# Kernel optimization log

Hardware: AMD Instinct MI355X
Metric: run time of the kernel (lower is better)

The kernel has to match this reference:

```python
import jax, jax.numpy as jnp
import numpy as np

EPS = 1e-6
N_HEADS, N_POINTS = 6, 4


def layer_norm(x, w, b):
    m = jnp.mean(x, -1, keepdims=True)
    v = jnp.mean((x - m) ** 2, -1, keepdims=True)
    return (x - m) * jax.lax.rsqrt(v + EPS) * w + b


def bilinear_sample(val, loc, Hl, Wl):
    # val: (B, nH, Hl*Wl, d); loc: (B, Lq, nH, P, 2) in [0,1]
    # matches F.grid_sample(mode='bilinear', padding='zeros', align_corners=False)
    B, nH, _, d = val.shape
    Lq, P = loc.shape[1], loc.shape[3]
    x = loc[..., 0] * Wl - 0.5
    y = loc[..., 1] * Hl - 0.5
    x0 = jnp.floor(x)
    y0 = jnp.floor(y)
    wx1 = x - x0
    wy1 = y - y0
    out = jnp.zeros((B, nH, Lq * P, d), val.dtype)
    corners = ((0, 0, (1 - wy1) * (1 - wx1)), (0, 1, (1 - wy1) * wx1),
               (1, 0, wy1 * (1 - wx1)), (1, 1, wy1 * wx1))
    for dy, dx, w in corners:
        xi = x0 + dx
        yi = y0 + dy
        valid = (xi >= 0) & (xi < Wl) & (yi >= 0) & (yi < Hl)
        xi_c = jnp.clip(xi, 0, Wl - 1).astype(jnp.int32)
        yi_c = jnp.clip(yi, 0, Hl - 1).astype(jnp.int32)
        idx = (yi_c * Wl + xi_c).transpose(0, 2, 1, 3).reshape(B, nH, Lq * P)
        g = jnp.take_along_axis(val, idx[..., None], axis=2)  # (B,nH,Lq*P,d)
        ww = jnp.where(valid, w, 0.0).transpose(0, 2, 1, 3).reshape(B, nH, Lq * P)
        out = out + g * ww[..., None]
    return out.reshape(B, nH, Lq, P, d).transpose(0, 2, 1, 3, 4)  # (B,Lq,nH,P,d)


def dwconv3x3(x, w, b):
    # x: (N, C, H, W); w: (C, 1, 3, 3) depthwise
    y = jax.lax.conv_general_dilated(x, w, (1, 1), 'SAME',
                                     feature_group_count=w.shape[0],
                                     dimension_numbers=('NCHW', 'OIHW', 'NCHW'))
    return y + b[None, :, None, None]


def setup_inputs() -> dict:
    key = jax.random.key(0)
    ks = jax.random.split(key, 16)
    B, H, W, C = 8, 32, 32, 768
    Lq = 3 * H * W
    Hf = Wf = 64
    hidden = int(C * 0.25)
    s = 0.02
    inp = {
        'query': jax.random.normal(ks[0], (B, Lq, C), jnp.float32),
        'reference_points': jax.random.uniform(ks[1], (B, Lq, 1, 2), jnp.float32),
        'feat': jax.random.normal(ks[2], (B, Hf * Wf, C), jnp.float32),
        'spatial_shapes': jnp.array([[Hf, Wf]], jnp.int32),
        'level_start_index': jnp.zeros((1,), jnp.int32),
        'H': H, 'W': W,
        'qn_w': jnp.ones((C,)), 'qn_b': jnp.zeros((C,)),
        'fn_w': jnp.ones((C,)), 'fn_b': jnp.zeros((C,)),
        'so_w': jax.random.normal(ks[3], (C, N_HEADS * N_POINTS * 2)) * s,
        'so_b': jax.random.normal(ks[4], (N_HEADS * N_POINTS * 2,)) * s,
        'aw_w': jax.random.normal(ks[5], (C, N_HEADS * N_POINTS)) * s,
        'aw_b': jnp.zeros((N_HEADS * N_POINTS,)),
        'vp_w': jax.random.normal(ks[6], (C, C)) * s,
        'vp_b': jnp.zeros((C,)),
        'op_w': jax.random.normal(ks[7], (C, C)) * s,
        'op_b': jnp.zeros((C,)),
        'ffn_w': jnp.ones((C,)), 'ffn_b': jnp.zeros((C,)),
        'fc1_w': jax.random.normal(ks[8], (C, hidden)) * s,
        'fc1_b': jnp.zeros((hidden,)),
        'dw_w': jax.random.normal(ks[9], (hidden, 1, 3, 3)) * s,
        'dw_b': jnp.zeros((hidden,)),
        'fc2_w': jax.random.normal(ks[10], (hidden, C)) * s,
        'fc2_b': jnp.zeros((C,)),
    }
    return inp


def reference(query, reference_points, feat, spatial_shapes, level_start_index, H, W,
              qn_w, qn_b, fn_w, fn_b, so_w, so_b, aw_w, aw_b, vp_w, vp_b, op_w, op_b,
              ffn_w, ffn_b, fc1_w, fc1_b, dw_w, dw_b, fc2_w, fc2_b):
    B, Lq, C = query.shape
    nH, nP = N_HEADS, N_POINTS
    d = C // nH
    ss = np.asarray(spatial_shapes)
    Hl, Wl = int(ss[0, 0]), int(ss[0, 1])

    # --- MSDeformAttn (single level) ---
    q = layer_norm(query, qn_w, qn_b)
    f = layer_norm(feat, fn_w, fn_b)
    value = (f @ vp_w + vp_b).reshape(B, Hl * Wl, nH, d).transpose(0, 2, 1, 3)  # (B,nH,Lin,d)
    offs = (q @ so_w + so_b).reshape(B, Lq, nH, 1, nP, 2)
    aw = jax.nn.softmax((q @ aw_w + aw_b).reshape(B, Lq, nH, nP), axis=-1)
    normalizer = jnp.array([Wl, Hl], query.dtype)
    loc = reference_points[:, :, None, :, None, :] + offs / normalizer  # (B,Lq,nH,1,nP,2)
    sampled = bilinear_sample(value, loc[:, :, :, 0], Hl, Wl)           # (B,Lq,nH,nP,d)
    attn = (sampled * aw[..., None]).sum(3).reshape(B, Lq, C) @ op_w + op_b
    query = query + attn

    # --- ConvFFN (3 equal HxW chunks through shared depthwise conv) ---
    x = layer_norm(query, ffn_w, ffn_b) @ fc1_w + fc1_b  # (B, 3*H*W, hid)
    n = Lq // 3
    hid = fc1_w.shape[1]
    xc = x.reshape(B, 3, n, hid).transpose(0, 1, 3, 2).reshape(B * 3, hid, H, W)
    xc = dwconv3x3(xc, dw_w, dw_b)
    x = xc.reshape(B, 3, hid, n).transpose(0, 1, 3, 2).reshape(B, Lq, hid)
    x = jax.nn.gelu(x, approximate=False)
    x = x @ fc2_w + fc2_b
    return query + x
```

## Files before the change

### kernel.cpp

```cpp
#include <hip/hip_runtime.h>
#include <hip/hip_bf16.h>
#include <math.h>

typedef __hip_bfloat16 bf16;
typedef short bf16x8 __attribute__((ext_vector_type(8)));
typedef short bf16x4 __attribute__((ext_vector_type(4)));
typedef float f32x4 __attribute__((ext_vector_type(4)));

#define NB 8
#define LQ 3072
#define CC 768
#define NHEADS 6
#define NPTS 4
#define DHEAD 128
#define HLVL 64
#define WLVL 64
#define LIN 4096
#define HID 192
#define BLTOT 24576
#define FROWS 32768

__device__ __forceinline__ float bf2f(short u)
{ return __uint_as_float(((unsigned)(unsigned short)u) << 16); }

template<int N_>
__device__ __forceinline__ void wait_vmcnt()
{
    if constexpr (N_ == 0)      asm volatile("s_waitcnt vmcnt(0)" ::: "memory");
    else if constexpr (N_ == 2) asm volatile("s_waitcnt vmcnt(2)" ::: "memory");
    else if constexpr (N_ == 4) asm volatile("s_waitcnt vmcnt(4)" ::: "memory");
    else if constexpr (N_ == 6) asm volatile("s_waitcnt vmcnt(6)" ::: "memory");
    else if constexpr (N_ == 8) asm volatile("s_waitcnt vmcnt(8)" ::: "memory");
    else static_assert(N_ == 0, "add a vmcnt case");
}

__global__ __launch_bounds__(256)
void ln_f32_wave_kernel(const float* __restrict__ x, const float* __restrict__ w,
                        const float* __restrict__ b, bf16* __restrict__ out)
{
    const int row = blockIdx.x * 4 + (threadIdx.x >> 6);
    const int lane = threadIdx.x & 63;
    const f32x4* xr = (const f32x4*)(x + (size_t)row * CC);
    f32x4 f0 = xr[lane], f1 = xr[64 + lane], f2 = xr[128 + lane];
    float s = 0.f, ss = 0.f;
    #pragma unroll
    for (int k = 0; k < 4; ++k) {
        s += f0[k] + f1[k] + f2[k];
        ss += f0[k] * f0[k] + f1[k] * f1[k] + f2[k] * f2[k];
    }
    #pragma unroll
    for (int o = 32; o > 0; o >>= 1) { s += __shfl_down(s, o); ss += __shfl_down(ss, o); }
    s = __shfl(s, 0); ss = __shfl(ss, 0);
    const float m = s * (1.f / CC);
    const float rs = rsqrtf(ss * (1.f / CC) - m * m + 1e-6f);
    const f32x4* w4 = (const f32x4*)w;
    const f32x4* b4 = (const f32x4*)b;
    bf16* orow = out + (size_t)row * CC;
    #pragma unroll
    for (int j = 0; j < 3; ++j) {
        f32x4 fj = (j == 0) ? f0 : (j == 1) ? f1 : f2;
        f32x4 wj = w4[j * 64 + lane], bj = b4[j * 64 + lane];
        bf16 t4[4];
        #pragma unroll
        for (int k = 0; k < 4; ++k) t4[k] = __float2bfloat16((fj[k] - m) * rs * wj[k] + bj[k]);
        *(bf16x4*)(orow + j * 256 + lane * 4) = *(bf16x4*)t4;
    }
}

__global__ __launch_bounds__(256)
void wt_bf16_kernel(const float* __restrict__ src, bf16* __restrict__ dst, int K, int N)
{
    __shared__ float t[64][65];
    const int tn0 = blockIdx.x * 64, tk0 = blockIdx.y * 64;
    const int r = threadIdx.x >> 6, c = threadIdx.x & 63;
    #pragma unroll
    for (int i = 0; i < 16; ++i) {
        const int k = i * 4 + r;
        t[k][c] = src[(size_t)(tk0 + k) * N + tn0 + c];
    }
    __syncthreads();
    #pragma unroll
    for (int i = 0; i < 16; ++i) {
        const int n = i * 4 + r;
        dst[(size_t)(tn0 + n) * K + tk0 + c] = __float2bfloat16(t[c][n]);
    }
}

__global__ __launch_bounds__(256)
void build_dots_w(const float* __restrict__ so_w, const float* __restrict__ so_b,
                  const float* __restrict__ aw_w, const float* __restrict__ aw_b,
                  bf16* __restrict__ wt, float* __restrict__ db)
{
    int i = blockIdx.x * 256 + threadIdx.x;
    if (i < 128 * 768) {
        int n = i / 768, k = i - n * 768;
        float v = 0.f;
        if (n < 48) v = so_w[(size_t)k * 48 + n];
        else if (n < 72) v = aw_w[(size_t)k * 24 + (n - 48)];
        wt[i] = __float2bfloat16(v);
    }
    if (i < 128) {
        float bv = 0.f;
        if (i < 48) bv = so_b[i];
        else if (i < 72) bv = aw_b[i - 48];
        db[i] = bv;
    }
}

template<int BM, int BN, int WM, int WN, int MODE>
__global__ __launch_bounds__(256)
void gemm_kernel(const bf16* __restrict__ A, const bf16* __restrict__ Bt,
                 const float* __restrict__ bias, const void* __restrict__ resv,
                 void* __restrict__ outv, int M, int N, int K)
{
    constexpr int WAVES_N = BN / WN;
    constexpr int FM = WM / 16, FN = WN / 16;
    constexpr int CWA = BM / 32;
    constexpr int CWB = BN / 32;
    constexpr int LPT = CWA + CWB;
    constexpr int ABYTES = BM * 256;
    constexpr int DBUF_BYTES = (BM + BN) * 256;
    constexpr int EPI_BYTES = BM * BN * 4;
    constexpr size_t SMEM_BYTES = DBUF_BYTES > EPI_BYTES ? DBUF_BYTES : EPI_BYTES;
    __shared__ __align__(16) char smem[SMEM_BYTES];
    bf16* sA = (bf16*)smem;
    bf16* sB = (bf16*)(smem + ABYTES);
    float* epi = (float*)smem;

    const int tid = threadIdx.x;
    const int lane = tid & 63;
    const int wave = tid >> 6;

    const int nwgx = gridDim.x;
    const int nwg = nwgx * gridDim.y;
    const int bid = blockIdx.y * nwgx + blockIdx.x;
    const int swz = (bid & 7) * (nwg >> 3) + (bid >> 3);
    const int m0 = (swz / nwgx) * BM;
    const int n0 = (swz % nwgx) * BN;

    const int wm = (wave / WAVES_N) * WM;
    const int wn = (wave % WAVES_N) * WN;

    const int srow = lane >> 3;
    const int scol = ((lane & 7) ^ srow) * 8;

    constexpr int GPR8 = BN / 8;
    constexpr int GPT8 = (BM * BN / 8) / 256;
    constexpr int QPR4 = BN / 4;
    constexpr int QPT4 = (BM * BN / 4) / 256;
    float4 pr0[GPT8], pr1[GPT8];
    bf16x4 prb[QPT4];
    if constexpr (MODE == 3) {
        const float* resf = (const float*)resv;
        #pragma unroll
        for (int k = 0; k < GPT8; ++k) {
            const int f = k * 256 + tid;
            const int rr = f / GPR8, cc = (f % GPR8) * 8;
            const size_t gidx = (size_t)(m0 + rr) * N + n0 + cc;
            pr0[k] = *(const float4*)&resf[gidx];
            pr1[k] = *(const float4*)&resf[gidx + 4];
        }
    }
    if constexpr (MODE == 4) {
        const bf16* resb = (const bf16*)resv;
        #pragma unroll
        for (int k = 0; k < QPT4; ++k) {
            const int f = k * 256 + tid;
            const int rr = f / QPR4, cc = (f % QPR4) * 4;
            prb[k] = *(const bf16x4*)&resb[(size_t)(m0 + rr) * N + n0 + cc];
        }
    }

#define STAGE(tt, half)                                                                            \
    { const int k0_ = (tt) * 64;                                                                   \
      _Pragma("unroll")                                                                            \
      for (int i_ = 0; i_ < CWA; ++i_) {                                                           \
        const int c_ = i_ * 4 + wave;                                                              \
        __builtin_amdgcn_global_load_lds(                                                          \
          (const __attribute__((address_space(1))) void*)(A + (size_t)(m0 + c_ * 8 + srow) * K + k0_ + scol), \
          (__attribute__((address_space(3))) void*)(sA + (half) * (BM * 64) + c_ * 512), 16, 0, 0); } \
      _Pragma("unroll")                                                                            \
      for (int i_ = 0; i_ < CWB; ++i_) {                                                           \
        const int c_ = i_ * 4 + wave;                                                              \
        __builtin_amdgcn_global_load_lds(                                                          \
          (const __attribute__((address_space(1))) void*)(Bt + (size_t)(n0 + c_ * 8 + srow) * K + k0_ + scol), \
          (__attribute__((address_space(3))) void*)(sB + (half) * (BN * 64) + c_ * 512), 16, 0, 0); } }

    f32x4 acc[FM][FN] = {};
    const int nt = K >> 6;

    STAGE(0, 0);
    STAGE(1, 1);

    for (int t = 0; t < nt; ++t) {
        const int half = t & 1;
        if (t + 1 < nt) wait_vmcnt<LPT>();
        else            wait_vmcnt<0>();
        __builtin_amdgcn_s_barrier();
        const bf16* cA = sA + half * (BM * 64);
        const bf16* cB = sB + half * (BN * 64);
        #pragma unroll
        for (int kki = 0; kki < 2; ++kki) {
            const int kslot = kki * 4 + (lane >> 4);
            bf16x8 aF[FM], bF[FN];
            #pragma unroll
            for (int i = 0; i < FM; ++i) {
                const int row = wm + i * 16 + (lane & 15);
                aF[i] = *(const bf16x8*)(&cA[row * 64 + ((kslot ^ (row & 7)) * 8)]);
            }
            #pragma unroll
            for (int j = 0; j < FN; ++j) {
                const int row = wn + j * 16 + (lane & 15);
                bF[j] = *(const bf16x8*)(&cB[row * 64 + ((kslot ^ (row & 7)) * 8)]);
            }
            #pragma unroll
            for (int i = 0; i < FM; ++i) {
                #pragma unroll
                for (int j = 0; j < FN; ++j)
                    acc[i][j] = __builtin_amdgcn_mfma_f32_16x16x32_bf16(aF[i], bF[j], acc[i][j], 0, 0, 0);
            }
        }
        asm volatile("s_waitcnt lgkmcnt(0)" ::: "memory");
        __builtin_amdgcn_s_barrier();
        if (t + 2 < nt) STAGE(t + 2, half);
    }
#undef STAGE

    #pragma unroll
    for (int j = 0; j < FN; ++j) {
        const int colL = wn + j * 16 + (lane & 15);
        const float bj = bias[n0 + colL];
        #pragma unroll
        for (int i = 0; i < FM; ++i) {
            #pragma unroll
            for (int r = 0; r < 4; ++r) {
                const int rowL = wm + i * 16 + ((lane >> 4) << 2) + r;
                const int addr = rowL * BN + ((((colL >> 2) ^ (rowL & 7)) << 2) | (colL & 3));
                epi[addr] = acc[i][j][r] + bj;
            }
        }
    }
    __syncthreads();

    if constexpr (MODE == 0 || MODE == 3) {
        #pragma unroll
        for (int k = 0; k < GPT8; ++k) {
            const int f = k * 256 + tid;
            const int rr = f / GPR8, cc = (f % GPR8) * 8;
            const int g0 = ((cc >> 2) ^ (rr & 7)) << 2;
            const int g1 = (((cc >> 2) + 1) ^ (rr & 7)) << 2;
            float4 v0 = *(const float4*)&epi[rr * BN + g0];
            float4 v1 = *(const float4*)&epi[rr * BN + g1];
            if constexpr (MODE == 3) {
                v0.x += pr0[k].x; v0.y += pr0[k].y; v0.z += pr0[k].z; v0.w += pr0[k].w;
                v1.x += pr1[k].x; v1.y += pr1[k].y; v1.z += pr1[k].z; v1.w += pr1[k].w;
            }
            bf16 tmp[8];
            tmp[0] = __float2bfloat16(v0.x); tmp[1] = __float2bfloat16(v0.y);
            tmp[2] = __float2bfloat16(v0.z); tmp[3] = __float2bfloat16(v0.w);
            tmp[4] = __float2bfloat16(v1.x); tmp[5] = __float2bfloat16(v1.y);
            tmp[6] = __float2bfloat16(v1.z); tmp[7] = __float2bfloat16(v1.w);
            *(bf16x8*)((bf16*)outv + (size_t)(m0 + rr) * N + n0 + cc) = *(bf16x8*)tmp;
        }
    } else {
        #pragma unroll
        for (int k = 0; k < QPT4; ++k) {
            const int f = k * 256 + tid;
            const int rr = f / QPR4, cc = (f % QPR4) * 4;
            const int gs = ((cc >> 2) ^ (rr & 7)) << 2;
            float4 v = *(const float4*)&epi[rr * BN + gs];
            if constexpr (MODE == 4) {
                v.x += bf2f(prb[k][0]); v.y += bf2f(prb[k][1]);
                v.z += bf2f(prb[k][2]); v.w += bf2f(prb[k][3]);
            }
            *(float4*)&((float*)outv)[(size_t)(m0 + rr) * N + n0 + cc] = v;
        }
    }
}

template<int BM, int BN, int WM, int WN, bool F32IN, int EPI>
__global__ __launch_bounds__(256)
void ln_gemm_kernel(const void* __restrict__ xv, const float* __restrict__ lnw,
                    const float* __restrict__ lnb, const bf16* __restrict__ Bt,
                    const float* __restrict__ bias, const float* __restrict__ refp,
                    void* __restrict__ outv, int M, int N)
{
    constexpr int WAVES_N = BN / WN;
    constexpr int FM = WM / 16, FN = WN / 16;
    constexpr int CWB = BN / 32;
    constexpr int RPW = BM / 4;
    static_assert(BM * BN * 4 <= 2 * BN * 64 * 2, "epi must fit in sB");
    __shared__ __align__(16) bf16 sA[BM * 768];
    __shared__ __align__(16) char sBmem[2 * BN * 64 * 2];
    bf16* sB = (bf16*)sBmem;
    float* epi = (float*)sBmem;

    const int tid = threadIdx.x;
    const int lane = tid & 63;
    const int wave = tid >> 6;

    const int nwgx = gridDim.x;
    const int nwg = nwgx * gridDim.y;
    const int bid = blockIdx.y * nwgx + blockIdx.x;
    const int swz = (bid & 7) * (nwg >> 3) + (bid >> 3);
    const int m0 = (swz / nwgx) * BM;
    const int n0 = (swz % nwgx) * BN;

    const int wm = (wave / WAVES_N) * WM;
    const int wn = (wave % WAVES_N) * WN;
    const int srow = lane >> 3;
    const int scol = ((lane & 7) ^ srow) * 8;

#define STAGEB(tt, half)                                                                           \
    { const int k0_ = (tt) * 64;                                                                   \
      _Pragma("unroll")                                                                            \
      for (int i_ = 0; i_ < CWB; ++i_) {                                                           \
        const int c_ = i_ * 4 + wave;                                                              \
        __builtin_amdgcn_global_load_lds(                                                          \
          (const __attribute__((address_space(1))) void*)(Bt + (size_t)(n0 + c_ * 8 + srow) * 768 + k0_ + scol), \
          (__attribute__((address_space(3))) void*)(sB + (half) * (BN * 64) + c_ * 512), 16, 0, 0); } }

    STAGEB(0, 0);
    STAGEB(1, 1);

    if constexpr (F32IN) {
        const f32x4* w4 = (const f32x4*)lnw;
        const f32x4* b4 = (const f32x4*)lnb;
        f32x4 wv0 = w4[lane], wv1 = w4[64 + lane], wv2 = w4[128 + lane];
        f32x4 bv0 = b4[lane], bv1 = b4[64 + lane], bv2 = b4[128 + lane];
        for (int rr = 0; rr < RPW; ++rr) {
            const int r = wave * RPW + rr;
            const f32x4* xr = (const f32x4*)((const float*)xv + (size_t)(m0 + r) * 768);
            f32x4 f0 = xr[lane], f1 = xr[64 + lane], f2 = xr[128 + lane];
            float s = 0.f, ss = 0.f;
            #pragma unroll
            for (int k = 0; k < 4; ++k) {
                s += f0[k] + f1[k] + f2[k];
                ss += f0[k] * f0[k] + f1[k] * f1[k] + f2[k] * f2[k];
            }
            #pragma unroll
            for (int o = 32; o > 0; o >>= 1) { s += __shfl_down(s, o); ss += __shfl_down(ss, o); }
            s = __shfl(s, 0); ss = __shfl(ss, 0);
            const float mn = s * (1.f / 768);
            const float rs = rsqrtf(ss * (1.f / 768) - mn * mn + 1e-6f);
            const int rx7 = r & 7;
            const int slot = (lane >> 1) & 7;
            const int off = (lane & 1) * 4;
            #pragma unroll
            for (int j = 0; j < 3; ++j) {
                f32x4 fj = (j == 0) ? f0 : (j == 1) ? f1 : f2;
                f32x4 wj = (j == 0) ? wv0 : (j == 1) ? wv1 : wv2;
                f32x4 bj = (j == 0) ? bv0 : (j == 1) ? bv1 : bv2;
                bf16 t4[4];
                #pragma unroll
                for (int k = 0; k < 4; ++k)
                    t4[k] = __float2bfloat16((fj[k] - mn) * rs * wj[k] + bj[k]);
                const int kt = j * 4 + (lane >> 4);
                *(bf16x4*)&sA[r * 768 + kt * 64 + ((slot ^ rx7) << 3) + off] = *(bf16x4*)t4;
            }
        }
    } else {
        const f32x4* w4 = (const f32x4*)lnw;
        const f32x4* b4 = (const f32x4*)lnb;
        f32x4 w80 = w4[lane * 2], w81 = w4[lane * 2 + 1], w44 = w4[128 + lane];
        f32x4 b80 = b4[lane * 2], b81 = b4[lane * 2 + 1], b44 = b4[128 + lane];
        for (int rr = 0; rr < RPW; ++rr) {
            const int r = wave * RPW + rr;
            const bf16* xr = (const bf16*)xv + (size_t)(m0 + r) * 768;
            bf16x8 v8 = *(const bf16x8*)(xr + lane * 8);
            bf16x4 v4 = *(const bf16x4*)(xr + 512 + lane * 4);
            float f[12];
            #pragma unroll
            for (int k = 0; k < 8; ++k) f[k] = bf2f(v8[k]);
            #pragma unroll
            for (int k = 0; k < 4; ++k) f[8 + k] = bf2f(v4[k]);
            float s = 0.f, ss = 0.f;
            #pragma unroll
            for (int k = 0; k < 12; ++k) { s += f[k]; ss += f[k] * f[k]; }
            #pragma unroll
            for (int o = 32; o > 0; o >>= 1) { s += __shfl_down(s, o); ss += __shfl_down(ss, o); }
            s = __shfl(s, 0); ss = __shfl(ss, 0);
            const float mn = s * (1.f / 768);
            const float rs = rsqrtf(ss * (1.f / 768) - mn * mn + 1e-6f);
            const int rx7 = r & 7;
            bf16 t8[8];
            #pragma unroll
            for (int k = 0; k < 4; ++k) t8[k] = __float2bfloat16((f[k] - mn) * rs * w80[k] + b80[k]);
            #pragma unroll
            for (int k = 0; k < 4; ++k) t8[4 + k] = __float2bfloat16((f[4 + k] - mn) * rs * w81[k] + b81[k]);
            *(bf16x8*)&sA[r * 768 + (lane >> 3) * 64 + (((lane & 7) ^ rx7) << 3)] = *(bf16x8*)t8;
            bf16 t4[4];
            #pragma unroll
            for (int k = 0; k < 4; ++k) t4[k] = __float2bfloat16((f[8 + k] - mn) * rs * w44[k] + b44[k]);
            *(bf16x4*)&sA[r * 768 + (8 + (lane >> 4)) * 64 + ((((lane >> 1) & 7) ^ rx7) << 3) + (lane & 1) * 4]
                = *(bf16x4*)t4;
        }
    }
    asm volatile("s_waitcnt lgkmcnt(0)" ::: "memory");

    f32x4 acc[FM][FN] = {};
    for (int t = 0; t < 12; ++t) {
        const int half = t & 1;
        if (t + 1 < 12) wait_vmcnt<CWB>();
        else            wait_vmcnt<0>();
        __builtin_amdgcn_s_barrier();
        const bf16* cB = sB + half * (BN * 64);
        #pragma unroll
        for (int kki = 0; kki < 2; ++kki) {
            const int kslot = kki * 4 + (lane >> 4);
            bf16x8 aF[FM], bF[FN];
            #pragma unroll
            for (int i = 0; i < FM; ++i) {
                const int row = wm + i * 16 + (lane & 15);
                aF[i] = *(const bf16x8*)(&sA[row * 768 + t * 64 + ((kslot ^ (row & 7)) * 8)]);
            }
            #pragma unroll
            for (int j = 0; j < FN; ++j) {
                const int row = wn + j * 16 + (lane & 15);
                bF[j] = *(const bf16x8*)(&cB[row * 64 + ((kslot ^ (row & 7)) * 8)]);
            }
            #pragma unroll
            for (int i = 0; i < FM; ++i) {
                #pragma unroll
                for (int j = 0; j < FN; ++j)
                    acc[i][j] = __builtin_amdgcn_mfma_f32_16x16x32_bf16(aF[i], bF[j], acc[i][j], 0, 0, 0);
            }
        }
        asm volatile("s_waitcnt lgkmcnt(0)" ::: "memory");
        __builtin_amdgcn_s_barrier();
        if (t + 2 < 12) STAGEB(t + 2, half);
    }
#undef STAGEB

    #pragma unroll
    for (int j = 0; j < FN; ++j) {
        const int colL = wn + j * 16 + (lane & 15);
        const float bj = bias[n0 + colL];
        #pragma unroll
        for (int i = 0; i < FM; ++i) {
            #pragma unroll
            for (int r = 0; r < 4; ++r) {
                const int rowL = wm + i * 16 + ((lane >> 4) << 2) + r;
                const int addr = rowL * BN + ((((colL >> 2) ^ (rowL & 7)) << 2) | (colL & 3));
                epi[addr] = acc[i][j][r] + bj;
            }
        }
    }
    __syncthreads();

    if constexpr (EPI == 1) {
        if (tid < BM * NHEADS) {
            const int rowL = tid & (BM - 1);
            const int h = tid / BM;
            auto erd = [&](int col) -> float {
                return epi[rowL * BN + ((((col >> 2) ^ (rowL & 7)) << 2) | (col & 3))];
            };
            float l0 = erd(48 + h * 4 + 0), l1 = erd(48 + h * 4 + 1);
            float l2 = erd(48 + h * 4 + 2), l3 = erd(48 + h * 4 + 3);
            float mx = fmaxf(fmaxf(l0, l1), fmaxf(l2, l3));
            float e0 = expf(l0 - mx), e1 = expf(l1 - mx), e2 = expf(l2 - mx), e3 = expf(l3 - mx);
            float inv = 1.f / (e0 + e1 + e2 + e3);
            float ee[4] = {e0, e1, e2, e3};
            const float rx = refp[(size_t)(m0 + rowL) * 2];
            const float ry = refp[(size_t)(m0 + rowL) * 2 + 1];
            float4* pp = (float4*)outv + ((size_t)(m0 + rowL) * NHEADS + h) * 4;
            #pragma unroll
            for (int p = 0; p < 4; ++p) {
                float ox = erd(h * 8 + p * 2), oy = erd(h * 8 + p * 2 + 1);
                pp[p] = make_float4(rx + ox * (1.f / WLVL), ry + oy * (1.f / HLVL), ee[p] * inv, 0.f);
            }
        }
    } else {
        constexpr int GPR8 = BN / 8;
        constexpr int GPT8 = (BM * BN / 8) / 256;
        #pragma unroll
        for (int k = 0; k < GPT8; ++k) {
            const int f = k * 256 + tid;
            const int rr = f / GPR8, cc = (f % GPR8) * 8;
            const int g0 = ((cc >> 2) ^ (rr & 7)) << 2;
            const int g1 = (((cc >> 2) + 1) ^ (rr & 7)) << 2;
            float4 v0 = *(const float4*)&epi[rr * BN + g0];
            float4 v1 = *(const float4*)&epi[rr * BN + g1];
            bf16 tmp[8];
            tmp[0] = __float2bfloat16(v0.x); tmp[1] = __float2bfloat16(v0.y);
            tmp[2] = __float2bfloat16(v0.z); tmp[3] = __float2bfloat16(v0.w);
            tmp[4] = __float2bfloat16(v1.x); tmp[5] = __float2bfloat16(v1.y);
            tmp[6] = __float2bfloat16(v1.z); tmp[7] = __float2bfloat16(v1.w);
            *(bf16x8*)((bf16*)outv + (size_t)(m0 + rr) * N + n0 + cc) = *(bf16x8*)tmp;
        }
    }
}

__global__ __launch_bounds__(256)
void sampler_kernel(const bf16* __restrict__ value, const float4* __restrict__ params,
                    bf16* __restrict__ attn_in)
{
    const int tid = threadIdx.x;
    const int cpx = gridDim.x >> 3;
    const int gblk = (blockIdx.x & 7) * cpx + (blockIdx.x >> 3);
    const int g = gblk * 16 + (tid >> 4);
    const int lane16 = tid & 15;
    const int bl = g / NHEADS;
    const int h = g - bl * NHEADS;
    const int b = bl / LQ;
    const bf16* vh = value + (size_t)b * LIN * CC + h * DHEAD + lane16 * 8;

    int offs[16];
    float wgt[16];
    #pragma unroll
    for (int p = 0; p < NPTS; ++p) {
        float4 pr = params[(size_t)g * 4 + p];
        float x = pr.x * (float)WLVL - 0.5f;
        float y = pr.y * (float)HLVL - 0.5f;
        float x0f = floorf(x), y0f = floorf(y);
        float wx1 = x - x0f, wy1 = y - y0f;
        float wx0 = 1.f - wx1, wy0 = 1.f - wy1;
        int x0 = (int)x0f, y0 = (int)y0f;
        #pragma unroll
        for (int dy = 0; dy < 2; ++dy) {
            const int yi = y0 + dy;
            const int yc = min(max(yi, 0), HLVL - 1);
            const float wy = (dy ? wy1 : wy0) * ((yi >= 0 && yi < HLVL) ? pr.z : 0.f);
            #pragma unroll
            for (int dx = 0; dx < 2; ++dx) {
                const int xi = x0 + dx;
                const int xc = min(max(xi, 0), WLVL - 1);
                const int idx = p * 4 + dy * 2 + dx;
                offs[idx] = (yc * WLVL + xc) * CC;
                wgt[idx] = wy * (dx ? wx1 : wx0) * ((xi >= 0 && xi < WLVL) ? 1.f : 0.f);
            }
        }
    }
    bf16x8 v[16];
    #pragma unroll
    for (int i = 0; i < 16; ++i) v[i] = *(const bf16x8*)(vh + offs[i]);
    float acc[8] = {};
    #pragma unroll
    for (int i = 0; i < 16; ++i) {
        #pragma unroll
        for (int j = 0; j < 8; ++j)
            acc[j] += wgt[i] * bf2f(v[i][j]);
    }
    bf16 tmp[8];
    #pragma unroll
    for (int j = 0; j < 8; ++j) tmp[j] = __float2bfloat16(acc[j]);
    *(bf16x8*)(attn_in + (size_t)bl * CC + h * DHEAD + lane16 * 8) = *(bf16x8*)tmp;
}

__global__ __launch_bounds__(192)
void dwconv_gelu_kernel(const bf16* __restrict__ z, const float* __restrict__ dw_w,
                        const float* __restrict__ dw_b, bf16* __restrict__ g)
{
    const int tp = threadIdx.x / 48;
    const int tc = threadIdx.x % 48;
    const int m = blockIdx.x * 4 + tp;
    const int c = tc * 4;
    const int pix = m & 1023;
    const int h = pix >> 5, w = pix & 31;
    float acc[4];
    #pragma unroll
    for (int j = 0; j < 4; ++j) acc[j] = dw_b[c + j];
    #pragma unroll
    for (int dy = -1; dy <= 1; ++dy) {
        int hh2 = h + dy;
        if (hh2 < 0 || hh2 >= 32) continue;
        #pragma unroll
        for (int dx = -1; dx <= 1; ++dx) {
            int ww2 = w + dx;
            if (ww2 < 0 || ww2 >= 32) continue;
            bf16x4 vv = *(const bf16x4*)&z[(size_t)(m + dy * 32 + dx) * HID + c];
            #pragma unroll
            for (int j = 0; j < 4; ++j)
                acc[j] += bf2f(vv[j]) * dw_w[(c + j) * 9 + (dy + 1) * 3 + (dx + 1)];
        }
    }
    bf16 tmp[4];
    #pragma unroll
    for (int j = 0; j < 4; ++j) {
        float ge = acc[j] * 0.5f * (1.f + erff(acc[j] * 0.70710678118f));
        tmp[j] = __float2bfloat16(ge);
    }
    *(bf16x4*)&g[(size_t)m * HID + c] = *(bf16x4*)tmp;
}

extern "C" void kernel_launch(void* const* d_in, const int* in_sizes, int n_in,
                              void* d_out, int out_size, void* d_ws, size_t ws_size,
                              hipStream_t stream)
{
    const float* query = (const float*)d_in[0];
    const float* refp  = (const float*)d_in[1];
    const float* feat  = (const float*)d_in[2];
    const float* qn_w = (const float*)d_in[7];
    const float* qn_b = (const float*)d_in[8];
    const float* fn_w = (const float*)d_in[9];
    const float* fn_b = (const float*)d_in[10];
    const float* so_w = (const float*)d_in[11];
    const float* so_b = (const float*)d_in[12];
    const float* aw_w = (const float*)d_in[13];
    const float* aw_b = (const float*)d_in[14];
    const float* vp_w = (const float*)d_in[15];
    const float* vp_b = (const float*)d_in[16];
    const float* op_w = (const float*)d_in[17];
    const float* op_b = (const float*)d_in[18];
    const float* ffn_w = (const float*)d_in[19];
    const float* ffn_b = (const float*)d_in[20];
    const float* fc1_w = (const float*)d_in[21];
    const float* fc1_b = (const float*)d_in[22];
    const float* dw_w = (const float*)d_in[23];
    const float* dw_b = (const float*)d_in[24];
    const float* fc2_w = (const float*)d_in[25];
    const float* fc2_b = (const float*)d_in[26];
    float* out = (float*)d_out;

    if (ws_size < (size_t)125829632) return;
    char* ws = (char*)d_ws;
    bf16* vp_wt   = (bf16*)(ws + 0);
    bf16* op_wt   = (bf16*)(ws + 1179648);
    bf16* fc1_wt  = (bf16*)(ws + 2359296);
    bf16* fc2_wt  = (bf16*)(ws + 2654208);
    bf16* dots_wt = (bf16*)(ws + 2949120);
    float* dots_b = (float*)(ws + 3145728);
    char* paramsR = ws + 3146240;
    char* dotsR   = ws + 12583424;
    char* regA = ws + 25166336;
    char* regB = ws + 75497984;
    float4* params = (float4*)paramsR;
    bf16* g        = (bf16*)paramsR;
    bf16* z        = (bf16*)dotsR;
    bf16* f_ln    = (bf16*)regA;
    bf16* attn_in = (bf16*)regA;
    bf16* value = (bf16*)regB;
    bf16* s_bf  = (bf16*)regB;

    wt_bf16_kernel<<<dim3(12, 12), 256, 0, stream>>>(vp_w, vp_wt, 768, 768);
    wt_bf16_kernel<<<dim3(12, 12), 256, 0, stream>>>(op_w, op_wt, 768, 768);
    wt_bf16_kernel<<<dim3(3, 12), 256, 0, stream>>>(fc1_w, fc1_wt, 768, 192);
    wt_bf16_kernel<<<dim3(12, 3), 256, 0, stream>>>(fc2_w, fc2_wt, 192, 768);
    build_dots_w<<<384, 256, 0, stream>>>(so_w, so_b, aw_w, aw_b, dots_wt, dots_b);

    ln_gemm_kernel<32, 128, 16, 64, true, 1><<<dim3(1, BLTOT / 32), 256, 0, stream>>>(
        query, qn_w, qn_b, dots_wt, dots_b, refp, params, BLTOT, 128);
    ln_f32_wave_kernel<<<FROWS / 4, 256, 0, stream>>>(feat, fn_w, fn_b, f_ln);
    gemm_kernel<128, 128, 64, 64, 0><<<dim3(6, FROWS / 128), 256, 0, stream>>>(
        f_ln, vp_wt, vp_b, nullptr, value, FROWS, 768, 768);
    sampler_kernel<<<(BLTOT * NHEADS) / 16, 256, 0, stream>>>(value, params, attn_in);
    gemm_kernel<64, 128, 32, 64, 3><<<dim3(6, BLTOT / 64), 256, 0, stream>>>(
        attn_in, op_wt, op_b, query, s_bf, BLTOT, 768, 768);

    ln_gemm_kernel<32, 64, 32, 16, false, 0><<<dim3(3, BLTOT / 32), 256, 0, stream>>>(
        s_bf, ffn_w, ffn_b, fc1_wt, fc1_b, nullptr, z, BLTOT, HID);
    dwconv_gelu_kernel<<<BLTOT / 4, 192, 0, stream>>>(z, dw_w, dw_b, g);
    gemm_kernel<64, 128, 32, 64, 4><<<dim3(6, BLTOT / 64), 256, 0, stream>>>(
        g, fc2_wt, fc2_b, s_bf, out, BLTOT, 768, HID);
}
```

Measured before the change: 327.2 us.

## Merge prep kernels and add 128x256 tiled value-projection GEMM

Five weight-prep launches and the feat LayerNorm kernel become one prep kernel that dispatches on block index, which removes launch overhead. The value projection moves to a new 512-thread GEMM with 128x256 tiles, an XCD-aware block swizzle and a two-pass epilogue that stages results through LDS. The larger tile raises operand reuse but uses more registers and shared memory per block, which may lower occupancy. The ln_gemm K loop is also fully unrolled.

```diff
diff --git a/kernel.cpp b/kernel.cpp
--- a/kernel.cpp
+++ b/kernel.cpp
@@ -34,76 +34,81 @@
     else static_assert(N_ == 0, "add a vmcnt case");
 }
 
+__device__ __forceinline__ void wt_tile(float (*t)[65], const float* __restrict__ src,
+                                        bf16* __restrict__ dst, int K, int N, int tn0, int tk0)
+{
+    const int r = threadIdx.x >> 6, c = threadIdx.x & 63;
+    #pragma unroll
+    for (int i = 0; i < 16; ++i)
+        t[i * 4 + r][c] = src[(size_t)(tk0 + i * 4 + r) * N + tn0 + c];
+    __syncthreads();
+    #pragma unroll
+    for (int i = 0; i < 16; ++i)
+        dst[(size_t)(tn0 + i * 4 + r) * K + tk0 + c] = __float2bfloat16(t[c][i * 4 + r]);
+}
+
 __global__ __launch_bounds__(256)
-void ln_f32_wave_kernel(const float* __restrict__ x, const float* __restrict__ w,
-                        const float* __restrict__ b, bf16* __restrict__ out)
-{
-    const int row = blockIdx.x * 4 + (threadIdx.x >> 6);
-    const int lane = threadIdx.x & 63;
-    const f32x4* xr = (const f32x4*)(x + (size_t)row * CC);
-    f32x4 f0 = xr[lane], f1 = xr[64 + lane], f2 = xr[128 + lane];
-    float s = 0.f, ss = 0.f;
-    #pragma unroll
-    for (int k = 0; k < 4; ++k) {
-        s += f0[k] + f1[k] + f2[k];
-        ss += f0[k] * f0[k] + f1[k] * f1[k] + f2[k] * f2[k];
-    }
-    #pragma unroll
-    for (int o = 32; o > 0; o >>= 1) { s += __shfl_down(s, o); ss += __shfl_down(ss, o); }
-    s = __shfl(s, 0); ss = __shfl(ss, 0);
-    const float m = s * (1.f / CC);
-    const float rs = rsqrtf(ss * (1.f / CC) - m * m + 1e-6f);
-    const f32x4* w4 = (const f32x4*)w;
-    const f32x4* b4 = (const f32x4*)b;
-    bf16* orow = out + (size_t)row * CC;
-    #pragma unroll
-    for (int j = 0; j < 3; ++j) {
-        f32x4 fj = (j == 0) ? f0 : (j == 1) ? f1 : f2;
-        f32x4 wj = w4[j * 64 + lane], bj = b4[j * 64 + lane];
-        bf16 t4[4];
-        #pragma unroll
-        for (int k = 0; k < 4; ++k) t4[k] = __float2bfloat16((fj[k] - m) * rs * wj[k] + bj[k]);
-        *(bf16x4*)(orow + j * 256 + lane * 4) = *(bf16x4*)t4;
-    }
-}
-
-__global__ __launch_bounds__(256)
-void wt_bf16_kernel(const float* __restrict__ src, bf16* __restrict__ dst, int K, int N)
+void prep_kernel(const float* __restrict__ vp_w, const float* __restrict__ op_w,
+                 const float* __restrict__ fc1_w, const float* __restrict__ fc2_w,
+                 const float* __restrict__ so_w, const float* __restrict__ so_b,
+                 const float* __restrict__ aw_w, const float* __restrict__ aw_b,
+                 const float* __restrict__ feat, const float* __restrict__ fn_w,
+                 const float* __restrict__ fn_b,
+                 bf16* __restrict__ vp_wt, bf16* __restrict__ op_wt,
+                 bf16* __restrict__ fc1_wt, bf16* __restrict__ fc2_wt,
+                 bf16* __restrict__ dots_wt, float* __restrict__ db,
+                 bf16* __restrict__ f_ln)
 {
     __shared__ float t[64][65];
-    const int tn0 = blockIdx.x * 64, tk0 = blockIdx.y * 64;
-    const int r = threadIdx.x >> 6, c = threadIdx.x & 63;
-    #pragma unroll
-    for (int i = 0; i < 16; ++i) {
-        const int k = i * 4 + r;
-        t[k][c] = src[(size_t)(tk0 + k) * N + tn0 + c];
-    }
-    __syncthreads();
-    #pragma unroll
-    for (int i = 0; i < 16; ++i) {
-        const int n = i * 4 + r;
-        dst[(size_t)(tn0 + n) * K + tk0 + c] = __float2bfloat16(t[c][n]);
-    }
-}
-
-__global__ __launch_bounds__(256)
-void build_dots_w(const float* __restrict__ so_w, const float* __restrict__ so_b,
-                  const float* __restrict__ aw_w, const float* __restrict__ aw_b,
-                  bf16* __restrict__ wt, float* __restrict__ db)
-{
-    int i = blockIdx.x * 256 + threadIdx.x;
-    if (i < 128 * 768) {
-        int n = i / 768, k = i - n * 768;
-        float v = 0.f;
-        if (n < 48) v = so_w[(size_t)k * 48 + n];
-        else if (n < 72) v = aw_w[(size_t)k * 24 + (n - 48)];
-        wt[i] = __float2bfloat16(v);
-    }
-    if (i < 128) {
-        float bv = 0.f;
-        if (i < 48) bv = so_b[i];
-        else if (i < 72) bv = aw_b[i - 48];
-        db[i] = bv;
+    int b = blockIdx.x;
+    if (b < 144)      wt_tile(t, vp_w, vp_wt, 768, 768, (b % 12) * 64, (b / 12) * 64);
+    else if (b < 288) { b -= 144; wt_tile(t, op_w, op_wt, 768, 768, (b % 12) * 64, (b / 12) * 64); }
+    else if (b < 324) { b -= 288; wt_tile(t, fc1_w, fc1_wt, 768, 192, (b % 3) * 64, (b / 3) * 64); }
+    else if (b < 360) { b -= 324; wt_tile(t, fc2_w, fc2_wt, 192, 768, (b % 12) * 64, (b / 12) * 64); }
+    else if (b < 744) {
+        b -= 360;
+        int i = b * 256 + threadIdx.x;
+        if (i < 128 * 768) {
+            int n = i / 768, k = i - n * 768;
+            float v = 0.f;
+            if (n < 48) v = so_w[(size_t)k * 48 + n];
+            else if (n < 72) v = aw_w[(size_t)k * 24 + (n - 48)];
+            dots_wt[i] = __float2bfloat16(v);
+        }
+        if (i < 128) {
+            float bv = 0.f;
+            if (i < 48) bv = so_b[i];
+            else if (i < 72) bv = aw_b[i - 48];
+            db[i] = bv;
+        }
+    } else {
+        const int row = (b - 744) * 4 + (threadIdx.x >> 6);
+        const int lane = threadIdx.x & 63;
+        const f32x4* xr = (const f32x4*)(feat + (size_t)row * CC);
+        f32x4 f0 = xr[lane], f1 = xr[64 + lane], f2 = xr[128 + lane];
+        float s = 0.f, ss = 0.f;
+        #pragma unroll
+        for (int k = 0; k < 4; ++k) {
+            s += f0[k] + f1[k] + f2[k];
+            ss += f0[k] * f0[k] + f1[k] * f1[k] + f2[k] * f2[k];
+        }
+        #pragma unroll
+        for (int o = 32; o > 0; o >>= 1) { s += __shfl_down(s, o); ss += __shfl_down(ss, o); }
+        s = __shfl(s, 0); ss = __shfl(ss, 0);
+        const float m = s * (1.f / CC);
+        const float rs = rsqrtf(ss * (1.f / CC) - m * m + 1e-6f);
+        const f32x4* w4 = (const f32x4*)fn_w;
+        const f32x4* b4 = (const f32x4*)fn_b;
+        bf16* orow = f_ln + (size_t)row * CC;
+        #pragma unroll
+        for (int j = 0; j < 3; ++j) {
+            f32x4 fj = (j == 0) ? f0 : (j == 1) ? f1 : f2;
+            f32x4 wj = w4[j * 64 + lane], bj = b4[j * 64 + lane];
+            bf16 t4[4];
+            #pragma unroll
+            for (int k = 0; k < 4; ++k) t4[k] = __float2bfloat16((fj[k] - m) * rs * wj[k] + bj[k]);
+            *(bf16x4*)(orow + j * 256 + lane * 4) = *(bf16x4*)t4;
+        }
     }
 }
 
@@ -278,6 +283,128 @@
     }
 }
 
+__global__ __launch_bounds__(512)
+void gemm_value_kernel(const bf16* __restrict__ A, const bf16* __restrict__ Bt,
+                       const float* __restrict__ bias, bf16* __restrict__ outb,
+                       int M, int N, int K)
+{
+    constexpr int BM = 128, BN = 256;
+    constexpr int FM = 4, FN = 4;
+    constexpr int CWA = 2, CWB = 4;
+    constexpr int LPT = CWA + CWB;
+    __shared__ __align__(16) char smem[2 * (BM + BN) * 128];
+    bf16* sA = (bf16*)smem;
+    bf16* sB = (bf16*)(smem + 2 * BM * 128);
+    float* epi = (float*)smem;
+
+    const int tid = threadIdx.x;
+    const int lane = tid & 63;
+    const int wave = tid >> 6;
+
+    const int nwgx = gridDim.x;
+    const int nwg = nwgx * gridDim.y;
+    const int bid = blockIdx.y * nwgx + blockIdx.x;
+    const int swz = (bid & 7) * (nwg >> 3) + (bid >> 3);
+    const int m0 = (swz / nwgx) * BM;
+    const int n0 = (swz % nwgx) * BN;
+
+    const int wm = (wave >> 2) * 64;
+    const int wn = (wave & 3) * 64;
+    const int srow = lane >> 3;
+    const int scol = ((lane & 7) ^ srow) * 8;
+
+#define STAGEV(tt, half)                                                                           \
+    { const int k0_ = (tt) * 64;                                                                   \
+      _Pragma("unroll")                                                                            \
+      for (int i_ = 0; i_ < CWA; ++i_) {                                                           \
+        const int c_ = i_ * 8 + wave;                                                              \
+        __builtin_amdgcn_global_load_lds(                                                          \
+          (const __attribute__((address_space(1))) void*)(A + (size_t)(m0 + c_ * 8 + srow) * K + k0_ + scol), \
+          (__attribute__((address_space(3))) void*)(sA + (half) * (BM * 64) + c_ * 512), 16, 0, 0); } \
+      _Pragma("unroll")                                                                            \
+      for (int i_ = 0; i_ < CWB; ++i_) {                                                           \
+        const int c_ = i_ * 8 + wave;                                                              \
+        __builtin_amdgcn_global_load_lds(                                                          \
+          (const __attribute__((address_space(1))) void*)(Bt + (size_t)(n0 + c_ * 8 + srow) * K + k0_ + scol), \
+          (__attribute__((address_space(3))) void*)(sB + (half) * (BN * 64) + c_ * 512), 16, 0, 0); } }
+
+    f32x4 acc[FM][FN] = {};
+    const int nt = K >> 6;
+
+    STAGEV(0, 0);
+    STAGEV(1, 1);
+
+    for (int t = 0; t < nt; ++t) {
+        const int half = t & 1;
+        if (t + 1 < nt) wait_vmcnt<LPT>();
+        else            wait_vmcnt<0>();
+        __builtin_amdgcn_s_barrier();
+        const bf16* cA = sA + half * (BM * 64);
+        const bf16* cB = sB + half * (BN * 64);
+        #pragma unroll
+        for (int kki = 0; kki < 2; ++kki) {
+            const int kslot = kki * 4 + (lane >> 4);
+            bf16x8 aF[FM], bF[FN];
+            #pragma unroll
+            for (int i = 0; i < FM; ++i) {
+                const int row = wm + i * 16 + (lane & 15);
+                aF[i] = *(const bf16x8*)(&cA[row * 64 + ((kslot ^ (row & 7)) * 8)]);
+            }
+            #pragma unroll
+            for (int j = 0; j < FN; ++j) {
+                const int row = wn + j * 16 + (lane & 15);
+                bF[j] = *(const bf16x8*)(&cB[row * 64 + ((kslot ^ (row & 7)) * 8)]);
+            }
+            #pragma unroll
+            for (int i = 0; i < FM; ++i) {
+                #pragma unroll
+                for (int j = 0; j < FN; ++j)
+                    acc[i][j] = __builtin_amdgcn_mfma_f32_16x16x32_bf16(aF[i], bF[j], acc[i][j], 0, 0, 0);
+            }
+        }
+        asm volatile("s_waitcnt lgkmcnt(0)" ::: "memory");
+        __builtin_amdgcn_s_barrier();
+        if (t + 2 < nt) STAGEV(t + 2, half);
+    }
+#undef STAGEV
+
+    for (int half = 0; half < 2; ++half) {
+        if ((wave >> 2) == half) {
+            #pragma unroll
+            for (int j = 0; j < FN; ++j) {
+                const int colL = wn + j * 16 + (lane & 15);
+                const float bj = bias[n0 + colL];
+                #pragma unroll
+                for (int i = 0; i < FM; ++i) {
+                    #pragma unroll
+                    for (int r = 0; r < 4; ++r) {
+                        const int lr = i * 16 + ((lane >> 4) << 2) + r;
+                        const int addr = lr * BN + ((((colL >> 2) ^ (lr & 7)) << 2) | (colL & 3));
+                        epi[addr] = acc[i][j][r] + bj;
+                    }
+                }
+            }
+        }
+        __syncthreads();
+        #pragma unroll
+        for (int k = 0; k < 4; ++k) {
+            const int f = k * 512 + tid;
+            const int rr = f >> 5, cc = (f & 31) * 8;
+            const int g0 = ((cc >> 2) ^ (rr & 7)) << 2;
+            const int g1 = (((cc >> 2) + 1) ^ (rr & 7)) << 2;
+            float4 v0 = *(const float4*)&epi[rr * BN + g0];
+            float4 v1 = *(const float4*)&epi[rr * BN + g1];
+            bf16 tmp[8];
+            tmp[0] = __float2bfloat16(v0.x); tmp[1] = __float2bfloat16(v0.y);
+            tmp[2] = __float2bfloat16(v0.z); tmp[3] = __float2bfloat16(v0.w);
+            tmp[4] = __float2bfloat16(v1.x); tmp[5] = __float2bfloat16(v1.y);
+            tmp[6] = __float2bfloat16(v1.z); tmp[7] = __float2bfloat16(v1.w);
+            *(bf16x8*)(outb + (size_t)(m0 + half * 64 + rr) * N + n0 + cc) = *(bf16x8*)tmp;
+        }
+        __syncthreads();
+    }
+}
+
 template<int BM, int BN, int WM, int WN, bool F32IN, int EPI>
 __global__ __launch_bounds__(256)
 void ln_gemm_kernel(const void* __restrict__ xv, const float* __restrict__ lnw,
@@ -399,6 +526,7 @@
     asm volatile("s_waitcnt lgkmcnt(0)" ::: "memory");
 
     f32x4 acc[FM][FN] = {};
+    #pragma unroll
     for (int t = 0; t < 12; ++t) {
         const int half = t & 1;
         if (t + 1 < 12) wait_vmcnt<CWB>();
@@ -632,17 +760,14 @@
     bf16* value = (bf16*)regB;
     bf16* s_bf  = (bf16*)regB;
 
-    wt_bf16_kernel<<<dim3(12, 12), 256, 0, stream>>>(vp_w, vp_wt, 768, 768);
-    wt_bf16_kernel<<<dim3(12, 12), 256, 0, stream>>>(op_w, op_wt, 768, 768);
-    wt_bf16_kernel<<<dim3(3, 12), 256, 0, stream>>>(fc1_w, fc1_wt, 768, 192);
-    wt_bf16_kernel<<<dim3(12, 3), 256, 0, stream>>>(fc2_w, fc2_wt, 192, 768);
-    build_dots_w<<<384, 256, 0, stream>>>(so_w, so_b, aw_w, aw_b, dots_wt, dots_b);
+    prep_kernel<<<744 + FROWS / 4, 256, 0, stream>>>(
+        vp_w, op_w, fc1_w, fc2_w, so_w, so_b, aw_w, aw_b, feat, fn_w, fn_b,
+        vp_wt, op_wt, fc1_wt, fc2_wt, dots_wt, dots_b, f_ln);
 
     ln_gemm_kernel<32, 128, 16, 64, true, 1><<<dim3(1, BLTOT / 32), 256, 0, stream>>>(
         query, qn_w, qn_b, dots_wt, dots_b, refp, params, BLTOT, 128);
-    ln_f32_wave_kernel<<<FROWS / 4, 256, 0, stream>>>(feat, fn_w, fn_b, f_ln);
-    gemm_kernel<128, 128, 64, 64, 0><<<dim3(6, FROWS / 128), 256, 0, stream>>>(
-        f_ln, vp_wt, vp_b, nullptr, value, FROWS, 768, 768);
+    gemm_value_kernel<<<dim3(3, FROWS / 128), 512, 0, stream>>>(
+        f_ln, vp_wt, vp_b, value, FROWS, 768, 768);
     sampler_kernel<<<(BLTOT * NHEADS) / 16, 256, 0, stream>>>(value, params, attn_in);
     gemm_kernel<64, 128, 32, 64, 3><<<dim3(6, BLTOT / 64), 256, 0, stream>>>(
         attn_in, op_wt, op_b, query, s_bf, BLTOT, 768, 768);
```

New measurement: 308.1 us. 1.06x faster.
